# Kernel optimization log

Measured on AMD Instinct MI355X. Metric: run time of the kernel, lower is better.

## Reference

```python
import jax, jax.numpy as jnp
import numpy as np

ALPHA = 0.2  # LeakyReLU negative slope
NEG_INF = -1.0e12


def setup_inputs() -> dict:
    key = jax.random.key(0)
    k1, k2, k3, k4 = jax.random.split(key, 4)
    B, N, Fin, Fout = 4, 4096, 256, 128
    inp = jax.random.normal(k1, (B, N, Fin), dtype=jnp.float32)
    adj_weights = jax.random.uniform(k2, (B, N, N), dtype=jnp.float32)
    W = jax.random.normal(k3, (Fin, Fout), dtype=jnp.float32) * (1.414 / np.sqrt(Fin))
    a = jax.random.normal(k4, (2 * Fout, 1), dtype=jnp.float32) * 0.1
    return {"inp": inp, "adj_weights": adj_weights, "W": W, "a": a}


def reference(inp, adj_weights, W, a):
    Fout = W.shape[1]
    h = jnp.matmul(inp, W)                       # [B, N, Fout]
    # a_input[b,i,j] = concat(h[b,i], h[b,j]); matmul with a splits into two rank-1 terms
    a1 = a[:Fout, 0]                             # [Fout]
    a2 = a[Fout:, 0]                             # [Fout]
    s1 = jnp.einsum('bnf,f->bn', h, a1)          # [B, N]
    s2 = jnp.einsum('bnf,f->bn', h, a2)          # [B, N]
    e = jax.nn.leaky_relu(s1[:, :, None] + s2[:, None, :], negative_slope=ALPHA)  # [B,N,N]
    attention = jnp.where(adj_weights > 0, adj_weights * e, NEG_INF)
    attention = jax.nn.softmax(attention, axis=2)
    # dropout p=0.0 / eval mode -> identity
    h_prime = jnp.matmul(attention, h)           # [B, N, Fout]
    return jax.nn.elu(h_prime)                   # concat=True branch
```

## Files before the change

kernel.cpp:

```cpp
#include <hip/hip_runtime.h>
#include <math.h>

typedef float    float4_t __attribute__((ext_vector_type(4)));
typedef _Float16 half8    __attribute__((ext_vector_type(8)));
typedef _Float16 half4_t  __attribute__((ext_vector_type(4)));

__global__ __launch_bounds__(256) void k_prep(const float* __restrict__ inp,
                                              const float* __restrict__ W,
                                              const float* __restrict__ a,
                                              float* __restrict__ s1,
                                              float* __restrict__ s2,
                                              _Float16* __restrict__ hT) {
    __shared__ float sA[32 * 68];
    __shared__ float sW[64 * 128];
    const int t   = threadIdx.x;
    const int gr0 = blockIdx.x * 32;
    const int b   = gr0 >> 12;
    const int f0  = (t & 15) * 8;
    const int r0  = (t >> 4) * 2;
    float4_t acc0[2] = {}; float4_t acc1[2] = {};
    for (int kc = 0; kc < 4; ++kc) {
        __syncthreads();
        #pragma unroll
        for (int it = 0; it < 2; ++it) {
            int fi = it * 256 + t; int r = fi >> 4; int c = (fi & 15) * 4;
            *(float4_t*)&sA[r * 68 + c] =
                *(const float4_t*)&inp[(size_t)(gr0 + r) * 256 + kc * 64 + c];
        }
        #pragma unroll
        for (int it = 0; it < 8; ++it) {
            int fi = it * 256 + t; int k = fi >> 5; int c = (fi & 31) * 4;
            *(float4_t*)&sW[k * 128 + c] =
                *(const float4_t*)&W[(size_t)(kc * 64 + k) * 128 + c];
        }
        __syncthreads();
        for (int k = 0; k < 64; ++k) {
            float4_t w0 = *(const float4_t*)&sW[k * 128 + f0];
            float4_t w1 = *(const float4_t*)&sW[k * 128 + f0 + 4];
            #pragma unroll
            for (int r = 0; r < 2; ++r) {
                float av = sA[(r0 + r) * 68 + k];
                acc0[r] += av * w0; acc1[r] += av * w1;
            }
        }
    }
    float4_t a1lo = *(const float4_t*)&a[f0];
    float4_t a1hi = *(const float4_t*)&a[f0 + 4];
    float4_t a2lo = *(const float4_t*)&a[128 + f0];
    float4_t a2hi = *(const float4_t*)&a[128 + f0 + 4];
    #pragma unroll
    for (int r = 0; r < 2; ++r) {
        const int row  = gr0 + r0 + r;
        const int rloc = row & 4095;
        #pragma unroll
        for (int c = 0; c < 4; ++c) {
            hT[(size_t)b * (128 * 4096) + (size_t)(f0 + c) * 4096 + rloc]     = (_Float16)acc0[r][c];
            hT[(size_t)b * (128 * 4096) + (size_t)(f0 + 4 + c) * 4096 + rloc] = (_Float16)acc1[r][c];
        }
        float p1 = acc0[r][0]*a1lo[0] + acc0[r][1]*a1lo[1] + acc0[r][2]*a1lo[2] + acc0[r][3]*a1lo[3]
                 + acc1[r][0]*a1hi[0] + acc1[r][1]*a1hi[1] + acc1[r][2]*a1hi[2] + acc1[r][3]*a1hi[3];
        float p2 = acc0[r][0]*a2lo[0] + acc0[r][1]*a2lo[1] + acc0[r][2]*a2lo[2] + acc0[r][3]*a2lo[3]
                 + acc1[r][0]*a2hi[0] + acc1[r][1]*a2hi[1] + acc1[r][2]*a2hi[2] + acc1[r][3]*a2hi[3];
        #pragma unroll
        for (int o = 1; o < 16; o <<= 1) { p1 += __shfl_xor(p1, o); p2 += __shfl_xor(p2, o); }
        if ((t & 15) == 0) { s1[row] = p1; s2[row] = p2; }
    }
}

__global__ __launch_bounds__(256) void k_s2max(const float* __restrict__ s2,
                                               float* __restrict__ s2max) {
    const int b = blockIdx.x, t = threadIdx.x;
    float m = -INFINITY;
    for (int i = t; i < 4096; i += 256) m = fmaxf(m, s2[b * 4096 + i]);
    #pragma unroll
    for (int o = 1; o < 64; o <<= 1) m = fmaxf(m, __shfl_xor(m, o));
    __shared__ float sm[4];
    if ((t & 63) == 0) sm[t >> 6] = m;
    __syncthreads();
    if (t == 0) s2max[b] = fmaxf(fmaxf(sm[0], sm[1]), fmaxf(sm[2], sm[3]));
}

__global__ __launch_bounds__(256, 4) void k_flash(const float* __restrict__ adj,
                                                  const _Float16* __restrict__ hT,
                                                  const float* __restrict__ s1,
                                                  const float* __restrict__ s2,
                                                  const float* __restrict__ s2max,
                                                  float* __restrict__ part_acc,
                                                  float* __restrict__ part_l) {
    __shared__ _Float16 hbuf[2][128 * 64];
    __shared__ _Float16 pbuf[4][16 * 64];

    const int t    = threadIdx.x;
    const int bid  = blockIdx.x;
    const int sp   = bid & 3;
    const int rb   = (bid >> 2) & 63;
    const int b    = bid >> 8;
    const int w    = t >> 6, lane = t & 63;
    const int quad = lane >> 4, ln15 = lane & 15;
    const int g    = quad;
    const int cl   = ln15;
    const int rowb = rb * 64 + w * 16;
    const float*    adj_w = adj + (size_t)b * 4096 * 4096 + (size_t)rowb * 4096;
    const _Float16* hT_b  = hT + (size_t)b * 128 * 4096;
    const float*    s2_b  = s2 + b * 4096;
    const float     s2m   = s2max[b];
    const int jwbase = sp * 1024;

    float s1r[4], mh[4];
    #pragma unroll
    for (int L = 0; L < 4; ++L) {
        s1r[L] = s1[b * 4096 + rowb + L * 4 + g];
        mh[L]  = fmaxf(0.f, s1r[L] + s2m);
    }

    const int sf  = t >> 3;
    const int sc  = t & 7;
    const int fb7 = ln15 & 7;

    float4_t acc[8] = {};
    float4_t psacc = {0.f, 0.f, 0.f, 0.f};

    {
        half8 hreg[4];
        #pragma unroll
        for (int i = 0; i < 4; ++i) {
            int f = i * 32 + sf;
            hreg[i] = *(const half8*)&hT_b[(size_t)f * 4096 + jwbase + sc * 8];
        }
        #pragma unroll
        for (int i = 0; i < 4; ++i) {
            int f = i * 32 + sf;
            *(half8*)&hbuf[0][f * 64 + ((sc ^ (f & 7)) << 3)] = hreg[i];
        }
    }
    __syncthreads();

    for (int jt = 0; jt < 16; ++jt) {
        const int cur = jt & 1;
        const int j0  = jwbase + jt * 64;
        half8 hreg[4];
        if (jt < 15) {
            #pragma unroll
            for (int i = 0; i < 4; ++i) {
                int f = i * 32 + sf;
                hreg[i] = *(const half8*)&hT_b[(size_t)f * 4096 + j0 + 64 + sc * 8];
            }
        }
        float4_t av[4];
        #pragma unroll
        for (int L = 0; L < 4; ++L)
            av[L] = *(const float4_t*)&adj_w[(size_t)(L * 4 + g) * 4096 + j0 + cl * 4];
        float4_t s2v = *(const float4_t*)&s2_b[j0 + cl * 4];
        #pragma unroll
        for (int L = 0; L < 4; ++L) {
            half4_t qv;
            #pragma unroll
            for (int c = 0; c < 4; ++c) {
                float x = s1r[L] + s2v[c];
                float e = x > 0.f ? x : 0.2f * x;
                float p = av[L][c] > 0.f ? __expf(fmaf(av[L][c], e, -mh[L])) : 0.f;
                _Float16 q = (_Float16)p;
                qv[c] = q;
                psacc[L] += (float)q;
            }
            const int r     = L * 4 + g;
            const int c0    = cl * 4;
            const int chunk = (c0 >> 3) ^ (r & 7);
            *(half4_t*)&pbuf[w][r * 64 + chunk * 8 + (c0 & 7)] = qv;
        }
        asm volatile("s_waitcnt lgkmcnt(0)" ::: "memory");
        half8 afrag[2];
        #pragma unroll
        for (int kc = 0; kc < 2; ++kc) {
            const int chunk = ((kc << 2) + quad) ^ (ln15 & 7);
            afrag[kc] = *(const half8*)&pbuf[w][ln15 * 64 + chunk * 8];
        }
        #pragma unroll
        for (int nt = 0; nt < 8; ++nt) {
            #pragma unroll
            for (int kc = 0; kc < 2; ++kc) {
                const int fb = nt * 16 + ln15;
                half8 bfrag = *(const half8*)&hbuf[cur][fb * 64 + ((((kc << 2) + quad) ^ fb7) << 3)];
                acc[nt] = __builtin_amdgcn_mfma_f32_16x16x32_f16(afrag[kc], bfrag, acc[nt], 0, 0, 0);
            }
        }
        if (jt < 15) {
            #pragma unroll
            for (int i = 0; i < 4; ++i) {
                int f = i * 32 + sf;
                *(half8*)&hbuf[1 - cur][f * 64 + ((sc ^ (f & 7)) << 3)] = hreg[i];
            }
        }
        __syncthreads();
    }
    #pragma unroll
    for (int o = 1; o < 16; o <<= 1) {
        #pragma unroll
        for (int L = 0; L < 4; ++L) psacc[L] += __shfl_xor(psacc[L], o);
    }
    const size_t growb = (size_t)b * 4096 + rowb;
    if (cl == 0) {
        #pragma unroll
        for (int L = 0; L < 4; ++L)
            part_l[(size_t)sp * 16384 + growb + L * 4 + g] = psacc[L];
    }
    float* pacc = part_acc + (size_t)sp * 16384 * 128;
    #pragma unroll
    for (int nt = 0; nt < 8; ++nt) {
        #pragma unroll
        for (int reg = 0; reg < 4; ++reg) {
            pacc[(growb + quad * 4 + reg) * 128 + nt * 16 + ln15] = acc[nt][reg];
        }
    }
}

__global__ __launch_bounds__(256) void k_combine(const float* __restrict__ part_acc,
                                                 const float* __restrict__ part_l,
                                                 float* __restrict__ out) {
    const int idx = blockIdx.x * 256 + threadIdx.x;
    const int e0  = idx * 4;
    const int gr  = e0 >> 7;
    float l = part_l[gr] + part_l[16384 + gr] + part_l[32768 + gr] + part_l[49152 + gr];
    float4_t a0 = *(const float4_t*)&part_acc[e0];
    float4_t a1 = *(const float4_t*)&part_acc[2097152 + e0];
    float4_t a2 = *(const float4_t*)&part_acc[4194304 + e0];
    float4_t a3 = *(const float4_t*)&part_acc[6291456 + e0];
    float4_t s  = (a0 + a1) + (a2 + a3);
    float rl = 1.f / l;
    float4_t o;
    #pragma unroll
    for (int c = 0; c < 4; ++c) {
        float v = s[c] * rl;
        o[c] = v > 0.f ? v : expm1f(v);
    }
    *(float4_t*)&((float*)out)[e0] = o;
}

extern "C" void kernel_launch(void* const* d_in, const int* in_sizes, int n_in,
                              void* d_out, int out_size, void* d_ws, size_t ws_size,
                              hipStream_t stream) {
    const float* inp = (const float*)d_in[0];
    const float* adj = (const float*)d_in[1];
    const float* W   = (const float*)d_in[2];
    const float* a   = (const float*)d_in[3];
    float* out = (float*)d_out;

    char* wsb = (char*)d_ws;
    _Float16* hT       = (_Float16*)(wsb);
    float*    s1       = (float*)(wsb + 4194304);
    float*    s2       = (float*)(wsb + 4259840);
    float*    s2max    = (float*)(wsb + 4325376);
    float*    part_l   = (float*)(wsb + 4325632);
    float*    part_acc = (float*)(wsb + 4587776);

    hipLaunchKernelGGL(k_prep,    dim3(512),  dim3(256), 0, stream, inp, W, a, s1, s2, hT);
    hipLaunchKernelGGL(k_s2max,   dim3(4),    dim3(256), 0, stream, s2, s2max);
    hipLaunchKernelGGL(k_flash,   dim3(1024), dim3(256), 0, stream, adj, hT, s1, s2, s2max,
                       part_acc, part_l);
    hipLaunchKernelGGL(k_combine, dim3(2048), dim3(256), 0, stream, part_acc, part_l, out);
}
```

Baseline: 435.1 us.

## Load h B-fragments directly from global memory, drop LDS staging and barriers

The flash kernel no longer stages the transposed h tile in a double-buffered LDS array with per-iteration __syncthreads. Each lane now reads its MFMA B-fragments straight from global/L2, double-buffered in registers across the nt loop. The adjacency and s2 loads are also software-pipelined one tile ahead. This cuts LDS usage and block barriers, which may allow higher occupancy, but every wave now re-reads h from global memory, so the kernel depends more on L2 bandwidth and latency.

```diff
diff --git a/kernel.cpp b/kernel.cpp
--- a/kernel.cpp
+++ b/kernel.cpp
@@ -87,7 +87,6 @@
                                                   const float* __restrict__ s2max,
                                                   float* __restrict__ part_acc,
                                                   float* __restrict__ part_l) {
-    __shared__ _Float16 hbuf[2][128 * 64];
     __shared__ _Float16 pbuf[4][16 * 64];
 
     const int t    = threadIdx.x;
@@ -113,44 +112,20 @@
         mh[L]  = fmaxf(0.f, s1r[L] + s2m);
     }
 
-    const int sf  = t >> 3;
-    const int sc  = t & 7;
-    const int fb7 = ln15 & 7;
+    const _Float16* hT_lane = hT_b + (size_t)ln15 * 4096 + (quad << 3);
 
     float4_t acc[8] = {};
     float4_t psacc = {0.f, 0.f, 0.f, 0.f};
 
-    {
-        half8 hreg[4];
-        #pragma unroll
-        for (int i = 0; i < 4; ++i) {
-            int f = i * 32 + sf;
-            hreg[i] = *(const half8*)&hT_b[(size_t)f * 4096 + jwbase + sc * 8];
-        }
-        #pragma unroll
-        for (int i = 0; i < 4; ++i) {
-            int f = i * 32 + sf;
-            *(half8*)&hbuf[0][f * 64 + ((sc ^ (f & 7)) << 3)] = hreg[i];
-        }
-    }
-    __syncthreads();
+    float4_t av[4];
+    float4_t s2v;
+    #pragma unroll
+    for (int L = 0; L < 4; ++L)
+        av[L] = *(const float4_t*)&adj_w[(size_t)(L * 4 + g) * 4096 + jwbase + cl * 4];
+    s2v = *(const float4_t*)&s2_b[jwbase + cl * 4];
 
     for (int jt = 0; jt < 16; ++jt) {
-        const int cur = jt & 1;
-        const int j0  = jwbase + jt * 64;
-        half8 hreg[4];
-        if (jt < 15) {
-            #pragma unroll
-            for (int i = 0; i < 4; ++i) {
-                int f = i * 32 + sf;
-                hreg[i] = *(const half8*)&hT_b[(size_t)f * 4096 + j0 + 64 + sc * 8];
-            }
-        }
-        float4_t av[4];
-        #pragma unroll
-        for (int L = 0; L < 4; ++L)
-            av[L] = *(const float4_t*)&adj_w[(size_t)(L * 4 + g) * 4096 + j0 + cl * 4];
-        float4_t s2v = *(const float4_t*)&s2_b[j0 + cl * 4];
+        const int j0 = jwbase + jt * 64;
         #pragma unroll
         for (int L = 0; L < 4; ++L) {
             half4_t qv;
@@ -168,6 +143,15 @@
             const int chunk = (c0 >> 3) ^ (r & 7);
             *(half4_t*)&pbuf[w][r * 64 + chunk * 8 + (c0 & 7)] = qv;
         }
+        if (jt < 15) {
+            #pragma unroll
+            for (int L = 0; L < 4; ++L)
+                av[L] = *(const float4_t*)&adj_w[(size_t)(L * 4 + g) * 4096 + j0 + 64 + cl * 4];
+            s2v = *(const float4_t*)&s2_b[j0 + 64 + cl * 4];
+        }
+        half8 bf[2][2];
+        bf[0][0] = *(const half8*)&hT_lane[j0];
+        bf[0][1] = *(const half8*)&hT_lane[j0 + 32];
         asm volatile("s_waitcnt lgkmcnt(0)" ::: "memory");
         half8 afrag[2];
         #pragma unroll
@@ -177,21 +161,14 @@
         }
         #pragma unroll
         for (int nt = 0; nt < 8; ++nt) {
-            #pragma unroll
-            for (int kc = 0; kc < 2; ++kc) {
-                const int fb = nt * 16 + ln15;
-                half8 bfrag = *(const half8*)&hbuf[cur][fb * 64 + ((((kc << 2) + quad) ^ fb7) << 3)];
-                acc[nt] = __builtin_amdgcn_mfma_f32_16x16x32_f16(afrag[kc], bfrag, acc[nt], 0, 0, 0);
+            const int cb = nt & 1;
+            if (nt < 7) {
+                bf[cb ^ 1][0] = *(const half8*)&hT_lane[(size_t)(nt + 1) * 16 * 4096 + j0];
+                bf[cb ^ 1][1] = *(const half8*)&hT_lane[(size_t)(nt + 1) * 16 * 4096 + j0 + 32];
             }
-        }
-        if (jt < 15) {
-            #pragma unroll
-            for (int i = 0; i < 4; ++i) {
-                int f = i * 32 + sf;
-                *(half8*)&hbuf[1 - cur][f * 64 + ((sc ^ (f & 7)) << 3)] = hreg[i];
-            }
-        }
-        __syncthreads();
+            acc[nt] = __builtin_amdgcn_mfma_f32_16x16x32_f16(afrag[0], bf[cb][0], acc[nt], 0, 0, 0);
+            acc[nt] = __builtin_amdgcn_mfma_f32_16x16x32_f16(afrag[1], bf[cb][1], acc[nt], 0, 0, 0);
+        }
     }
     #pragma unroll
     for (int o = 1; o < 16; o <<= 1) {
```

Result: slower. 476.7 us (+9.6%).

## Software-pipeline adj loads and P computation one tile ahead of MFMA

Applied to the files above, without the earlier changes.

Restructures the flash loop so the attention probabilities for tile jt+1 are computed into a double-buffered per-wave P buffer while the MFMAs for tile jt run, and the adjacency and s2 loads are issued two tiles ahead. This hides global load latency for adj behind the matrix work instead of stalling each iteration. It replaces __syncthreads with an explicit lgkmcnt wait plus s_barrier and lowers launch bounds occupancy from 4 to 3 blocks per CU to give room for the extra live registers. The cost is more LDS, higher register pressure and fewer resident waves to hide latency.

```diff
diff --git a/kernel.cpp b/kernel.cpp
--- a/kernel.cpp
+++ b/kernel.cpp
@@ -80,7 +80,7 @@
     if (t == 0) s2max[b] = fmaxf(fmaxf(sm[0], sm[1]), fmaxf(sm[2], sm[3]));
 }
 
-__global__ __launch_bounds__(256, 4) void k_flash(const float* __restrict__ adj,
+__global__ __launch_bounds__(256, 3) void k_flash(const float* __restrict__ adj,
                                                   const _Float16* __restrict__ hT,
                                                   const float* __restrict__ s1,
                                                   const float* __restrict__ s2,
@@ -88,7 +88,7 @@
                                                   float* __restrict__ part_acc,
                                                   float* __restrict__ part_l) {
     __shared__ _Float16 hbuf[2][128 * 64];
-    __shared__ _Float16 pbuf[4][16 * 64];
+    __shared__ _Float16 pbuf[4][2][16 * 64];
 
     const int t    = threadIdx.x;
     const int bid  = blockIdx.x;
@@ -119,38 +119,10 @@
 
     float4_t acc[8] = {};
     float4_t psacc = {0.f, 0.f, 0.f, 0.f};
-
-    {
-        half8 hreg[4];
-        #pragma unroll
-        for (int i = 0; i < 4; ++i) {
-            int f = i * 32 + sf;
-            hreg[i] = *(const half8*)&hT_b[(size_t)f * 4096 + jwbase + sc * 8];
-        }
-        #pragma unroll
-        for (int i = 0; i < 4; ++i) {
-            int f = i * 32 + sf;
-            *(half8*)&hbuf[0][f * 64 + ((sc ^ (f & 7)) << 3)] = hreg[i];
-        }
-    }
-    __syncthreads();
-
-    for (int jt = 0; jt < 16; ++jt) {
-        const int cur = jt & 1;
-        const int j0  = jwbase + jt * 64;
-        half8 hreg[4];
-        if (jt < 15) {
-            #pragma unroll
-            for (int i = 0; i < 4; ++i) {
-                int f = i * 32 + sf;
-                hreg[i] = *(const half8*)&hT_b[(size_t)f * 4096 + j0 + 64 + sc * 8];
-            }
-        }
-        float4_t av[4];
-        #pragma unroll
-        for (int L = 0; L < 4; ++L)
-            av[L] = *(const float4_t*)&adj_w[(size_t)(L * 4 + g) * 4096 + j0 + cl * 4];
-        float4_t s2v = *(const float4_t*)&s2_b[j0 + cl * 4];
+    float4_t av[4];
+    float4_t s2v;
+
+    auto pcompute = [&](int slot) {
         #pragma unroll
         for (int L = 0; L < 4; ++L) {
             half4_t qv;
@@ -166,14 +138,53 @@
             const int r     = L * 4 + g;
             const int c0    = cl * 4;
             const int chunk = (c0 >> 3) ^ (r & 7);
-            *(half4_t*)&pbuf[w][r * 64 + chunk * 8 + (c0 & 7)] = qv;
-        }
-        asm volatile("s_waitcnt lgkmcnt(0)" ::: "memory");
+            *(half4_t*)&pbuf[w][slot][r * 64 + chunk * 8 + (c0 & 7)] = qv;
+        }
+    };
+
+    {
+        half8 hreg[4];
+        #pragma unroll
+        for (int i = 0; i < 4; ++i) {
+            int f = i * 32 + sf;
+            hreg[i] = *(const half8*)&hT_b[(size_t)f * 4096 + jwbase + sc * 8];
+        }
+        #pragma unroll
+        for (int L = 0; L < 4; ++L)
+            av[L] = *(const float4_t*)&adj_w[(size_t)(L * 4 + g) * 4096 + jwbase + cl * 4];
+        s2v = *(const float4_t*)&s2_b[jwbase + cl * 4];
+        #pragma unroll
+        for (int i = 0; i < 4; ++i) {
+            int f = i * 32 + sf;
+            *(half8*)&hbuf[0][f * 64 + ((sc ^ (f & 7)) << 3)] = hreg[i];
+        }
+        pcompute(0);
+        #pragma unroll
+        for (int L = 0; L < 4; ++L)
+            av[L] = *(const float4_t*)&adj_w[(size_t)(L * 4 + g) * 4096 + jwbase + 64 + cl * 4];
+        s2v = *(const float4_t*)&s2_b[jwbase + 64 + cl * 4];
+    }
+    asm volatile("s_waitcnt lgkmcnt(0)" ::: "memory");
+    __builtin_amdgcn_s_barrier();
+
+    #pragma unroll 1
+    for (int jt = 0; jt < 16; ++jt) {
+        const int cur = jt & 1;
+        const int j0  = jwbase + jt * 64;
+        half8 hreg[4];
+        const bool tail = (jt == 15);
+        if (!tail) {
+            #pragma unroll
+            for (int i = 0; i < 4; ++i) {
+                int f = i * 32 + sf;
+                hreg[i] = *(const half8*)&hT_b[(size_t)f * 4096 + j0 + 64 + sc * 8];
+            }
+        }
         half8 afrag[2];
         #pragma unroll
         for (int kc = 0; kc < 2; ++kc) {
             const int chunk = ((kc << 2) + quad) ^ (ln15 & 7);
-            afrag[kc] = *(const half8*)&pbuf[w][ln15 * 64 + chunk * 8];
+            afrag[kc] = *(const half8*)&pbuf[w][cur][ln15 * 64 + chunk * 8];
         }
         #pragma unroll
         for (int nt = 0; nt < 8; ++nt) {
@@ -184,15 +195,24 @@
                 acc[nt] = __builtin_amdgcn_mfma_f32_16x16x32_f16(afrag[kc], bfrag, acc[nt], 0, 0, 0);
             }
         }
-        if (jt < 15) {
+        if (!tail) pcompute(cur ^ 1);
+        if (jt < 14) {
+            #pragma unroll
+            for (int L = 0; L < 4; ++L)
+                av[L] = *(const float4_t*)&adj_w[(size_t)(L * 4 + g) * 4096 + j0 + 128 + cl * 4];
+            s2v = *(const float4_t*)&s2_b[j0 + 128 + cl * 4];
+        }
+        if (!tail) {
             #pragma unroll
             for (int i = 0; i < 4; ++i) {
                 int f = i * 32 + sf;
-                *(half8*)&hbuf[1 - cur][f * 64 + ((sc ^ (f & 7)) << 3)] = hreg[i];
-            }
-        }
-        __syncthreads();
-    }
+                *(half8*)&hbuf[cur ^ 1][f * 64 + ((sc ^ (f & 7)) << 3)] = hreg[i];
+            }
+            asm volatile("s_waitcnt lgkmcnt(0)" ::: "memory");
+            __builtin_amdgcn_s_barrier();
+        }
+    }
+
     #pragma unroll
     for (int o = 1; o < 16; o <<= 1) {
         #pragma unroll
```

After: 446.4 us. +2.6%, slower.

## Stream adj and hT tiles into LDS via async global_load_lds double buffering

Applied to the files above, without the earlier changes.

Replaces register-staged loads of hT and direct global loads of adj with async global_load_lds DMA into double-buffered LDS, using vmcnt waits and raw barriers to overlap the next tile's fetch with current compute. s2 is also preloaded once into LDS. LDS use grows, so launch_bounds occupancy hint drops from 4 to 2 blocks per CU, which may reduce latency hiding from other waves.

```diff
diff --git a/kernel.cpp b/kernel.cpp
--- a/kernel.cpp
+++ b/kernel.cpp
@@ -4,6 +4,10 @@
 typedef float    float4_t __attribute__((ext_vector_type(4)));
 typedef _Float16 half8    __attribute__((ext_vector_type(8)));
 typedef _Float16 half4_t  __attribute__((ext_vector_type(4)));
+
+#define GLL16(G, L) __builtin_amdgcn_global_load_lds(                        \
+    (const __attribute__((address_space(1))) unsigned int*)(G),              \
+    (__attribute__((address_space(3))) unsigned int*)(L), 16, 0, 0)
 
 __global__ __launch_bounds__(256) void k_prep(const float* __restrict__ inp,
                                               const float* __restrict__ W,
@@ -80,7 +84,7 @@
     if (t == 0) s2max[b] = fmaxf(fmaxf(sm[0], sm[1]), fmaxf(sm[2], sm[3]));
 }
 
-__global__ __launch_bounds__(256, 4) void k_flash(const float* __restrict__ adj,
+__global__ __launch_bounds__(256, 2) void k_flash(const float* __restrict__ adj,
                                                   const _Float16* __restrict__ hT,
                                                   const float* __restrict__ s1,
                                                   const float* __restrict__ s2,
@@ -88,7 +92,9 @@
                                                   float* __restrict__ part_acc,
                                                   float* __restrict__ part_l) {
     __shared__ _Float16 hbuf[2][128 * 64];
+    __shared__ float    adjbuf[4][2][16 * 64];
     __shared__ _Float16 pbuf[4][16 * 64];
+    __shared__ float    s2buf[1024];
 
     const int t    = threadIdx.x;
     const int bid  = blockIdx.x;
@@ -102,9 +108,9 @@
     const int rowb = rb * 64 + w * 16;
     const float*    adj_w = adj + (size_t)b * 4096 * 4096 + (size_t)rowb * 4096;
     const _Float16* hT_b  = hT + (size_t)b * 128 * 4096;
-    const float*    s2_b  = s2 + b * 4096;
     const float     s2m   = s2max[b];
     const int jwbase = sp * 1024;
+    const int fb7 = ln15 & 7;
 
     float s1r[4], mh[4];
     #pragma unroll
@@ -113,52 +119,51 @@
         mh[L]  = fmaxf(0.f, s1r[L] + s2m);
     }
 
-    const int sf  = t >> 3;
-    const int sc  = t & 7;
-    const int fb7 = ln15 & 7;
+    *(float4_t*)&s2buf[t * 4] = *(const float4_t*)&s2[(size_t)b * 4096 + jwbase + t * 4];
+    asm volatile("s_waitcnt lgkmcnt(0)" ::: "memory");
 
     float4_t acc[8] = {};
     float4_t psacc = {0.f, 0.f, 0.f, 0.f};
 
-    {
-        half8 hreg[4];
+    auto stage = [&](int slot, int j0) {
         #pragma unroll
         for (int i = 0; i < 4; ++i) {
-            int f = i * 32 + sf;
-            hreg[i] = *(const half8*)&hT_b[(size_t)f * 4096 + jwbase + sc * 8];
+            const int r = i * 4 + (lane >> 4);
+            GLL16(adj_w + (size_t)r * 4096 + j0 + ((lane & 15) << 2),
+                  &adjbuf[w][slot][i * 256]);
         }
         #pragma unroll
         for (int i = 0; i < 4; ++i) {
-            int f = i * 32 + sf;
-            *(half8*)&hbuf[0][f * 64 + ((sc ^ (f & 7)) << 3)] = hreg[i];
-        }
-    }
-    __syncthreads();
-
+            const int f0r = (w * 4 + i) * 8;
+            const int f   = f0r + (lane >> 3);
+            const int sch = (lane & 7) ^ (f & 7);
+            GLL16(hT_b + ((size_t)f << 12) + j0 + (sch << 3),
+                  &hbuf[slot][f0r * 64]);
+        }
+    };
+
+    asm volatile("" ::: "memory");
+    stage(0, jwbase);
+
+    #pragma unroll 1
     for (int jt = 0; jt < 16; ++jt) {
         const int cur = jt & 1;
         const int j0  = jwbase + jt * 64;
-        half8 hreg[4];
-        if (jt < 15) {
-            #pragma unroll
-            for (int i = 0; i < 4; ++i) {
-                int f = i * 32 + sf;
-                hreg[i] = *(const half8*)&hT_b[(size_t)f * 4096 + j0 + 64 + sc * 8];
-            }
-        }
-        float4_t av[4];
-        #pragma unroll
-        for (int L = 0; L < 4; ++L)
-            av[L] = *(const float4_t*)&adj_w[(size_t)(L * 4 + g) * 4096 + j0 + cl * 4];
-        float4_t s2v = *(const float4_t*)&s2_b[j0 + cl * 4];
+        if (jt < 15) stage(cur ^ 1, j0 + 64);
+        if (jt < 15) asm volatile("s_waitcnt vmcnt(8)" ::: "memory");
+        else         asm volatile("s_waitcnt vmcnt(0)" ::: "memory");
+        __builtin_amdgcn_s_barrier();
+        asm volatile("" ::: "memory");
         #pragma unroll
         for (int L = 0; L < 4; ++L) {
+            float4_t av  = *(const float4_t*)&adjbuf[w][cur][(L * 4 + g) * 64 + cl * 4];
+            float4_t s2v = *(const float4_t*)&s2buf[jt * 64 + cl * 4];
             half4_t qv;
             #pragma unroll
             for (int c = 0; c < 4; ++c) {
                 float x = s1r[L] + s2v[c];
                 float e = x > 0.f ? x : 0.2f * x;
-                float p = av[L][c] > 0.f ? __expf(fmaf(av[L][c], e, -mh[L])) : 0.f;
+                float p = av[c] > 0.f ? __expf(fmaf(av[c], e, -mh[L])) : 0.f;
                 _Float16 q = (_Float16)p;
                 qv[c] = q;
                 psacc[L] += (float)q;
@@ -185,14 +190,11 @@
             }
         }
         if (jt < 15) {
-            #pragma unroll
-            for (int i = 0; i < 4; ++i) {
-                int f = i * 32 + sf;
-                *(half8*)&hbuf[1 - cur][f * 64 + ((sc ^ (f & 7)) << 3)] = hreg[i];
-            }
-        }
-        __syncthreads();
-    }
+            asm volatile("" ::: "memory");
+            __builtin_amdgcn_s_barrier();
+        }
+    }
+
     #pragma unroll
     for (int o = 1; o < 16; o <<= 1) {
         #pragma unroll
```

After: 429.7 us. Within noise of the previous version (-1.2%).
